# Kernel optimization log

Hardware: AMD Instinct MI355X
Metric: run time of the kernel (lower is better)

The kernel has to match this reference:

```python
import jax, jax.numpy as jnp
import numpy as np

_J6 = jnp.array([[0,0,0,0,0,1],[0,0,0,0,-1,0],[0,0,0,1,0,0],[0,0,1,0,0,0],[0,-1,0,0,0,0],[1,0,0,0,0,0]], dtype=jnp.float32)
# pairs (i,j) from combinations(range(4),2)
_PI = jnp.array([0,0,0,1,1,2])
_PJ = jnp.array([1,2,3,2,3,3])

def exterior(p1, p2):
    # p1, p2: [B,T,H,4] -> Plucker line coords [B,T,H,6], L2-normalized
    L = p1[..., _PI] * p2[..., _PJ] - p1[..., _PJ] * p2[..., _PI]
    n = jnp.clip(jnp.linalg.norm(L, axis=-1, keepdims=True), 1e-12)
    return L / n

def setup_inputs() -> dict:
    key = jax.random.key(0)
    ks = jax.random.split(key, 8)
    B, T, D, H = 2, 2048, 1024, 16
    pd = 4
    s = 0.02
    return {
        "x": jax.random.normal(ks[0], (B, T, D), jnp.float32),
        "w_qkv": jax.random.normal(ks[1], (3 * D, D), jnp.float32) * s,
        "b_qkv": jnp.zeros((3 * D,), jnp.float32),
        "w1_write": jax.random.normal(ks[2], (pd * H, D), jnp.float32) * s,
        "w2_write": jax.random.normal(ks[3], (pd * H, D), jnp.float32) * s,
        "w1_read": jax.random.normal(ks[4], (pd * H, D), jnp.float32) * s,
        "w2_read": jax.random.normal(ks[5], (pd * H, D), jnp.float32) * s,
        "w_out": jax.random.normal(ks[6], (D, D), jnp.float32) * s,
        "b_out": jnp.zeros((D,), jnp.float32),
        "decay_logits": jnp.full((H,), 4.6, jnp.float32),
        "bias_scale": jnp.full((H,), 0.1, jnp.float32),
    }

def reference(x, w_qkv, b_qkv, w1_write, w2_write, w1_read, w2_read, w_out, b_out, decay_logits, bias_scale):
    B, T, D = x.shape
    H = decay_logits.shape[0]
    dh = D // H
    pd = w1_write.shape[0] // H
    scale = dh ** -0.5

    qkv = (x @ w_qkv.T + b_qkv).reshape(B, T, 3, H, dh)
    qkv = jnp.transpose(qkv, (2, 0, 3, 1, 4))  # [3,B,H,T,dh]
    q, k, v = qkv[0], qkv[1], qkv[2]
    std_logits = jnp.einsum('bhqd,bhkd->bhqk', q, k) * scale

    x_prev = jnp.concatenate([jnp.zeros((B, 1, D), x.dtype), x[:, :-1]], axis=1)
    w1 = (x_prev @ w1_write.T).reshape(B, T, H, pd)
    w2 = (x @ w2_write.T).reshape(B, T, H, pd)
    write_lines = exterior(w1, w2)  # [B,T,H,6]
    r1 = (x @ w1_read.T).reshape(B, T, H, pd)
    r2 = (x @ w2_read.T).reshape(B, T, H, pd)
    read_lines = exterior(r1, r2)

    J_write = jnp.einsum('bthi,ij->bthj', write_lines, _J6)
    incidence = jnp.einsum('bqhp,bkhp->bhqk', read_lines, J_write)  # [B,H,T,T]

    decays = jax.nn.sigmoid(decay_logits)  # [H]
    pos = jnp.arange(T, dtype=x.dtype)
    diffs = pos[:, None] - pos[None, :]  # [T,T], q - k
    past = diffs > 0
    diffs_pos = jnp.where(past, diffs, 0.0)
    weights = (decays[:, None, None] ** diffs_pos[None]) * past[None].astype(x.dtype)  # [H,T,T]

    bias = incidence * weights[None] * bias_scale[None, :, None, None]
    logits = std_logits + bias
    causal_mask = diffs < 0  # k > q -> masked
    logits = jnp.where(causal_mask[None, None], -jnp.inf, logits)
    attn = jax.nn.softmax(logits, axis=-1)
    out = jnp.einsum('bhqk,bhkd->bqhd', attn, v).reshape(B, T, D)
    return out @ w_out.T + b_out
```

## Files before the change

kernel.cpp:

```cpp
#include <hip/hip_runtime.h>
#include <hip/hip_bf16.h>

using bhalf = __hip_bfloat16;
typedef __bf16 bf16x8 __attribute__((ext_vector_type(8)));
typedef float f32x4 __attribute__((ext_vector_type(4)));

#define B_DIM 2
#define T_DIM 2048
#define D_DIM 1024
#define H_DIM 16
#define DH 64

struct bh8 { bhalf v[8]; };
struct bh4 { bhalf v[4]; };

__device__ __forceinline__ bf16x8 load_bf16x8(const bhalf* p) {
    return __builtin_bit_cast(bf16x8, *(const uint4*)p);
}
__device__ __forceinline__ bf16x8 zero_bf16x8() {
    uint4 z; z.x = 0; z.y = 0; z.z = 0; z.w = 0;
    return __builtin_bit_cast(bf16x8, z);
}
__device__ __forceinline__ void stage8_cvt(bhalf* dst, const float* src) {
    float4 a = *(const float4*)src;
    float4 b = *(const float4*)(src + 4);
    bh8 t;
    t.v[0] = __float2bfloat16(a.x); t.v[1] = __float2bfloat16(a.y);
    t.v[2] = __float2bfloat16(a.z); t.v[3] = __float2bfloat16(a.w);
    t.v[4] = __float2bfloat16(b.x); t.v[5] = __float2bfloat16(b.y);
    t.v[6] = __float2bfloat16(b.z); t.v[7] = __float2bfloat16(b.w);
    *(uint4*)dst = __builtin_bit_cast(uint4, t);
}

#define GLD16(gp, lp) __builtin_amdgcn_global_load_lds( \
    (const __attribute__((address_space(1))) void*)(gp), \
    (__attribute__((address_space(3))) void*)(lp), 16, 0, 0)

#define SX  4194304
#define SW  3145728
#define SL  65536
#define SO  1048576
__global__ __launch_bounds__(256) void cvt_all(
    const float* __restrict__ x, const float* __restrict__ wqkv,
    const float* __restrict__ w1w, const float* __restrict__ w2w,
    const float* __restrict__ w1r, const float* __restrict__ w2r,
    const float* __restrict__ wout,
    bhalf* __restrict__ xbf, bhalf* __restrict__ wcat, bhalf* __restrict__ woutbf)
{
    int i = (blockIdx.x * 256 + threadIdx.x) * 8;
    if (i < SX) { stage8_cvt(xbf + i, x + i); return; }
    i -= SX;
    if (i < SW) { stage8_cvt(wcat + i, wqkv + i); return; }
    i -= SW;
    if (i < SL) { stage8_cvt(wcat + SW + i, w1w + i); return; }
    i -= SL;
    if (i < SL) { stage8_cvt(wcat + SW + SL + i, w2w + i); return; }
    i -= SL;
    if (i < SL) { stage8_cvt(wcat + SW + 2 * SL + i, w1r + i); return; }
    i -= SL;
    if (i < SL) { stage8_cvt(wcat + SW + 3 * SL + i, w2r + i); return; }
    i -= SL;
    if (i < SO) { stage8_cvt(woutbf + i, wout + i); }
}

__device__ __forceinline__ void gemm128_mainloop(
    const bhalf* __restrict__ A, const bhalf* __restrict__ B, int K,
    bhalf* As, bhalf* Bs, f32x4 acc[4][4])
{
    const int tid = threadIdx.x;
    const int wave = tid >> 6, lane = tid & 63;
    const int ln = lane & 15, lg = lane >> 4;
    const int wr = (wave >> 1) * 64, wc = (wave & 1) * 64;
    const int lrow = lane >> 3;
    const int lcol = (lane & 7) * 8;

    for (int kt = 0; kt < K; kt += 64) {
        __syncthreads();
#pragma unroll
        for (int i = 0; i < 4; ++i) {
            int idx = __builtin_amdgcn_readfirstlane(wave * 4 + i);
            GLD16(A + (size_t)(idx * 8 + lrow) * K + kt + lcol, As + idx * 512);
            GLD16(B + (size_t)(idx * 8 + lrow) * K + kt + lcol, Bs + idx * 512);
        }
        __syncthreads();
#pragma unroll
        for (int ks = 0; ks < 2; ++ks) {
            bf16x8 af[4], bfr[4];
#pragma unroll
            for (int mt = 0; mt < 4; ++mt)
                af[mt] = load_bf16x8(As + (wr + mt * 16 + ln) * 64 + ks * 32 + lg * 8);
#pragma unroll
            for (int nt = 0; nt < 4; ++nt)
                bfr[nt] = load_bf16x8(Bs + (wc + nt * 16 + ln) * 64 + ks * 32 + lg * 8);
#pragma unroll
            for (int mt = 0; mt < 4; ++mt)
#pragma unroll
                for (int nt = 0; nt < 4; ++nt)
                    acc[mt][nt] = __builtin_amdgcn_mfma_f32_16x16x32_bf16(af[mt], bfr[nt], acc[mt][nt], 0, 0, 0);
        }
    }
}

__global__ __launch_bounds__(256) void qkv_lines_gemm128(
    const bhalf* __restrict__ x, const bhalf* __restrict__ wcat, const float* __restrict__ bqkv,
    bhalf* __restrict__ qo, bhalf* __restrict__ ko, bhalf* __restrict__ vt,
    float* __restrict__ proj)
{
    __shared__ bhalf As[128 * 64];
    __shared__ bhalf Bs[128 * 64];
    f32x4 acc[4][4] = {};
    gemm128_mainloop(x + (size_t)blockIdx.x * 128 * D_DIM,
                     wcat + (size_t)blockIdx.y * 128 * D_DIM, D_DIM, As, Bs, acc);
    const int wave = threadIdx.x >> 6, lane = threadIdx.x & 63;
    const int ln = lane & 15, lg = lane >> 4;
    const int wr = (wave >> 1) * 64, wc = (wave & 1) * 64;
#pragma unroll
    for (int nt = 0; nt < 4; ++nt) {
        int n = blockIdx.y * 128 + wc + nt * 16 + ln;
        int trip = n >> 10, h = (n >> 6) & 15, d = n & 63;
        float bias = (trip < 3) ? bqkv[n] : 0.f;
#pragma unroll
        for (int mt = 0; mt < 4; ++mt)
#pragma unroll
            for (int r = 0; r < 4; ++r) {
                int tok = blockIdx.x * 128 + wr + mt * 16 + lg * 4 + r;
                int b = tok >> 11, t = tok & (T_DIM - 1);
                float y = acc[mt][nt][r] + bias;
                if (trip == 0) {
                    qo[(((size_t)(b * H_DIM + h)) * T_DIM + t) * DH + d] = __float2bfloat16(y * 0.125f);
                } else if (trip == 1) {
                    ko[(((size_t)(b * H_DIM + h)) * T_DIM + t) * DH + d] = __float2bfloat16(y);
                } else if (trip == 2) {
                    vt[(((size_t)(b * H_DIM + h)) * DH + d) * T_DIM + t] = __float2bfloat16(y);
                } else {
                    proj[(size_t)tok * 256 + (n - 3072)] = y;
                }
            }
    }
}

__global__ __launch_bounds__(256) void out_gemm64(
    const bhalf* __restrict__ a, const bhalf* __restrict__ w, const float* __restrict__ bo,
    float* __restrict__ out)
{
    __shared__ bhalf As[64 * 64];
    __shared__ bhalf Bs[64 * 64];
    const int tid = threadIdx.x;
    const int wave = tid >> 6, lane = tid & 63;
    const int ln = lane & 15, lg = lane >> 4;
    const int lrow = lane >> 3;
    const int lcol = (lane & 7) * 8;
    const bhalf* A = a + (size_t)blockIdx.x * 64 * D_DIM;
    const bhalf* B = w + (size_t)blockIdx.y * 64 * D_DIM;
    f32x4 acc[4] = {};

    for (int kt = 0; kt < D_DIM; kt += 64) {
        __syncthreads();
#pragma unroll
        for (int i = 0; i < 2; ++i) {
            int idx = __builtin_amdgcn_readfirstlane(wave * 2 + i);
            GLD16(A + (size_t)(idx * 8 + lrow) * D_DIM + kt + lcol, As + idx * 512);
            GLD16(B + (size_t)(idx * 8 + lrow) * D_DIM + kt + lcol, Bs + idx * 512);
        }
        __syncthreads();
#pragma unroll
        for (int ks = 0; ks < 2; ++ks) {
            bf16x8 af = load_bf16x8(As + (wave * 16 + ln) * 64 + ks * 32 + lg * 8);
#pragma unroll
            for (int nt = 0; nt < 4; ++nt) {
                bf16x8 bfr = load_bf16x8(Bs + (nt * 16 + ln) * 64 + ks * 32 + lg * 8);
                acc[nt] = __builtin_amdgcn_mfma_f32_16x16x32_bf16(af, bfr, acc[nt], 0, 0, 0);
            }
        }
    }
#pragma unroll
    for (int nt = 0; nt < 4; ++nt) {
        int n = blockIdx.y * 64 + nt * 16 + ln;
        float bias = bo[n];
#pragma unroll
        for (int r = 0; r < 4; ++r) {
            int tok = blockIdx.x * 64 + wave * 16 + lg * 4 + r;
            out[(size_t)tok * D_DIM + n] = acc[nt][r] + bias;
        }
    }
}

__global__ __launch_bounds__(256) void build_lines(
    const float* __restrict__ proj, const float* __restrict__ bias_scale,
    const float* __restrict__ decay_logits,
    bhalf* __restrict__ read8, bhalf* __restrict__ jw8)
{
    int id = blockIdx.x * 256 + threadIdx.x;
    int tok = id >> 4, h = id & 15;
    int b = tok >> 11, t = tok & (T_DIM - 1);
    const float* pr = proj + (size_t)tok * 256;

    float p1[4], p2[4], r1[4], r2[4];
#pragma unroll
    for (int i = 0; i < 4; ++i) {
        p1[i] = (t > 0) ? pr[-256 + h * 4 + i] : 0.f;
        p2[i] = pr[64 + h * 4 + i];
        r1[i] = pr[128 + h * 4 + i];
        r2[i] = pr[192 + h * 4 + i];
    }
    float Lw[6], Lr[6];
    {
        Lw[0] = p1[0] * p2[1] - p1[1] * p2[0];
        Lw[1] = p1[0] * p2[2] - p1[2] * p2[0];
        Lw[2] = p1[0] * p2[3] - p1[3] * p2[0];
        Lw[3] = p1[1] * p2[2] - p1[2] * p2[1];
        Lw[4] = p1[1] * p2[3] - p1[3] * p2[1];
        Lw[5] = p1[2] * p2[3] - p1[3] * p2[2];
        float n2 = 0.f;
#pragma unroll
        for (int j = 0; j < 6; ++j) n2 += Lw[j] * Lw[j];
        float inv = 1.f / fmaxf(sqrtf(n2), 1e-12f);
#pragma unroll
        for (int j = 0; j < 6; ++j) Lw[j] *= inv;
    }
    {
        Lr[0] = r1[0] * r2[1] - r1[1] * r2[0];
        Lr[1] = r1[0] * r2[2] - r1[2] * r2[0];
        Lr[2] = r1[0] * r2[3] - r1[3] * r2[0];
        Lr[3] = r1[1] * r2[2] - r1[2] * r2[1];
        Lr[4] = r1[1] * r2[3] - r1[3] * r2[1];
        Lr[5] = r1[2] * r2[3] - r1[3] * r2[2];
        float n2 = 0.f;
#pragma unroll
        for (int j = 0; j < 6; ++j) n2 += Lr[j] * Lr[j];
        float inv = 1.f / fmaxf(sqrtf(n2), 1e-12f);
#pragma unroll
        for (int j = 0; j < 6; ++j) Lr[j] *= inv;
    }
    float decay = 1.f / (1.f + __expf(-decay_logits[h]));
    float l2d = log2f(decay);
    float bs = bias_scale[h] * exp2f(-(float)t * l2d);
    size_t base = (((size_t)(b * H_DIM + h)) * T_DIM + t) * 8;
    read8[base + 0] = __float2bfloat16(Lr[0]);
    read8[base + 1] = __float2bfloat16(Lr[1]);
    read8[base + 2] = __float2bfloat16(Lr[2]);
    read8[base + 3] = __float2bfloat16(Lr[3]);
    read8[base + 4] = __float2bfloat16(Lr[4]);
    read8[base + 5] = __float2bfloat16(Lr[5]);
    read8[base + 6] = __float2bfloat16(0.f);
    read8[base + 7] = __float2bfloat16(0.f);
    jw8[base + 0] = __float2bfloat16(Lw[5] * bs);
    jw8[base + 1] = __float2bfloat16(-Lw[4] * bs);
    jw8[base + 2] = __float2bfloat16(Lw[3] * bs);
    jw8[base + 3] = __float2bfloat16(Lw[2] * bs);
    jw8[base + 4] = __float2bfloat16(-Lw[1] * bs);
    jw8[base + 5] = __float2bfloat16(Lw[0] * bs);
    jw8[base + 6] = __float2bfloat16(0.f);
    jw8[base + 7] = __float2bfloat16(0.f);
}

__global__ __launch_bounds__(256) void attn_kernel(
    const bhalf* __restrict__ q, const bhalf* __restrict__ k, const bhalf* __restrict__ vt,
    const bhalf* __restrict__ read8, const bhalf* __restrict__ jw8,
    const float* __restrict__ decay_logits, bhalf* __restrict__ attn_out)
{
    __shared__ float sm[4352];
    const int wave = threadIdx.x >> 6, lane = threadIdx.x & 63;
    const int ln = lane & 15, lg = lane >> 4;
    const int h = blockIdx.y, b = blockIdx.z;
    const int qa = blockIdx.x;
    const int qb = 127 - qa;
    const int rqa = qa * 16, rqb = qb * 16;
    const size_t hb = (size_t)(b * H_DIM + h);
    const bhalf* qh = q + hb * T_DIM * DH;
    const bhalf* kh = k + hb * T_DIM * DH;
    const bhalf* vh = vt + hb * DH * T_DIM;
    const bhalf* r8 = read8 + hb * T_DIM * 8;
    const bhalf* j8 = jw8 + hb * T_DIM * 8;

    bhalf* plA = (bhalf*)sm + wave * 640;
    bhalf* plB = (bhalf*)sm + 2560 + wave * 640;

    bf16x8 zf = zero_bf16x8();
    bf16x8 qA0 = load_bf16x8(qh + (rqa + ln) * DH + lg * 8);
    bf16x8 qA1 = load_bf16x8(qh + (rqa + ln) * DH + 32 + lg * 8);
    bf16x8 qB0 = load_bf16x8(qh + (rqb + ln) * DH + lg * 8);
    bf16x8 qB1 = load_bf16x8(qh + (rqb + ln) * DH + 32 + lg * 8);
    bf16x8 rfA = (lane < 16) ? load_bf16x8(r8 + (size_t)(rqa + ln) * 8) : zf;
    bf16x8 rfB = (lane < 16) ? load_bf16x8(r8 + (size_t)(rqb + ln) * 8) : zf;

    float decay = 1.f / (1.f + __expf(-decay_logits[h]));
    float l2d = log2f(decay);
    const float LOG2E = 1.44269504f;
    float aqA[4], aqB[4];
#pragma unroll
    for (int r = 0; r < 4; ++r) {
        aqA[r] = exp2f((float)(rqa + lg * 4 + r) * l2d);
        aqB[r] = exp2f((float)(rqb + lg * 4 + r) * l2d);
    }

    f32x4 oA[4] = {}, oB[4] = {};
    float lpA[4] = {0.f, 0.f, 0.f, 0.f}, lpB[4] = {0.f, 0.f, 0.f, 0.f};

    const int nca = qa / 2 + 1, ncb = qb / 2 + 1;
    for (int c = wave; c < ncb; c += 4) {
        const int kb = c * 32;
        bf16x8 k00 = load_bf16x8(kh + (kb + ln) * DH + lg * 8);
        bf16x8 k01 = load_bf16x8(kh + (kb + ln) * DH + 32 + lg * 8);
        bf16x8 k10 = load_bf16x8(kh + (kb + 16 + ln) * DH + lg * 8);
        bf16x8 k11 = load_bf16x8(kh + (kb + 16 + ln) * DH + 32 + lg * 8);
        bf16x8 j0 = (lane < 16) ? load_bf16x8(j8 + (size_t)(kb + ln) * 8) : zf;
        bf16x8 j1 = (lane < 16) ? load_bf16x8(j8 + (size_t)(kb + 16 + ln) * 8) : zf;
        bf16x8 vf0 = load_bf16x8(vh + (size_t)(ln) * T_DIM + kb + lg * 8);
        bf16x8 vf1 = load_bf16x8(vh + (size_t)(16 + ln) * T_DIM + kb + lg * 8);
        bf16x8 vf2 = load_bf16x8(vh + (size_t)(32 + ln) * T_DIM + kb + lg * 8);
        bf16x8 vf3 = load_bf16x8(vh + (size_t)(48 + ln) * T_DIM + kb + lg * 8);
        const bool doA = (c < nca);

        {
            f32x4 z0 = {}, z1 = {}, i0 = {}, i1 = {};
            z0 = __builtin_amdgcn_mfma_f32_16x16x32_bf16(qB0, k00, z0, 0, 0, 0);
            z0 = __builtin_amdgcn_mfma_f32_16x16x32_bf16(qB1, k01, z0, 0, 0, 0);
            i0 = __builtin_amdgcn_mfma_f32_16x16x32_bf16(rfB, j0, i0, 0, 0, 0);
            z1 = __builtin_amdgcn_mfma_f32_16x16x32_bf16(qB0, k10, z1, 0, 0, 0);
            z1 = __builtin_amdgcn_mfma_f32_16x16x32_bf16(qB1, k11, z1, 0, 0, 0);
            i1 = __builtin_amdgcn_mfma_f32_16x16x32_bf16(rfB, j1, i1, 0, 0, 0);
#pragma unroll
            for (int r = 0; r < 4; ++r) {
                int diff0 = rqb + lg * 4 + r - (kb + ln);
                float s0 = z0[r] + ((diff0 > 0) ? i0[r] * aqB[r] : 0.f);
                float p0 = (diff0 < 0) ? 0.f : exp2f(s0 * LOG2E);
                plB[(lg * 4 + r) * 40 + ln] = __float2bfloat16(p0);
                int diff1 = diff0 - 16;
                float s1 = z1[r] + ((diff1 > 0) ? i1[r] * aqB[r] : 0.f);
                float p1 = (diff1 < 0) ? 0.f : exp2f(s1 * LOG2E);
                plB[(lg * 4 + r) * 40 + 16 + ln] = __float2bfloat16(p1);
                lpB[r] += p0 + p1;
            }
        }
        if (doA) {
            f32x4 z0 = {}, z1 = {}, i0 = {}, i1 = {};
            z0 = __builtin_amdgcn_mfma_f32_16x16x32_bf16(qA0, k00, z0, 0, 0, 0);
            z0 = __builtin_amdgcn_mfma_f32_16x16x32_bf16(qA1, k01, z0, 0, 0, 0);
            i0 = __builtin_amdgcn_mfma_f32_16x16x32_bf16(rfA, j0, i0, 0, 0, 0);
            z1 = __builtin_amdgcn_mfma_f32_16x16x32_bf16(qA0, k10, z1, 0, 0, 0);
            z1 = __builtin_amdgcn_mfma_f32_16x16x32_bf16(qA1, k11, z1, 0, 0, 0);
            i1 = __builtin_amdgcn_mfma_f32_16x16x32_bf16(rfA, j1, i1, 0, 0, 0);
#pragma unroll
            for (int r = 0; r < 4; ++r) {
                int diff0 = rqa + lg * 4 + r - (kb + ln);
                float s0 = z0[r] + ((diff0 > 0) ? i0[r] * aqA[r] : 0.f);
                float p0 = (diff0 < 0) ? 0.f : exp2f(s0 * LOG2E);
                plA[(lg * 4 + r) * 40 + ln] = __float2bfloat16(p0);
                int diff1 = diff0 - 16;
                float s1 = z1[r] + ((diff1 > 0) ? i1[r] * aqA[r] : 0.f);
                float p1 = (diff1 < 0) ? 0.f : exp2f(s1 * LOG2E);
                plA[(lg * 4 + r) * 40 + 16 + ln] = __float2bfloat16(p1);
                lpA[r] += p0 + p1;
            }
        }
        __asm__ volatile("s_waitcnt lgkmcnt(0)" ::: "memory");
        {
            bf16x8 pf = load_bf16x8(plB + ln * 40 + lg * 8);
            oB[0] = __builtin_amdgcn_mfma_f32_16x16x32_bf16(pf, vf0, oB[0], 0, 0, 0);
            oB[1] = __builtin_amdgcn_mfma_f32_16x16x32_bf16(pf, vf1, oB[1], 0, 0, 0);
            oB[2] = __builtin_amdgcn_mfma_f32_16x16x32_bf16(pf, vf2, oB[2], 0, 0, 0);
            oB[3] = __builtin_amdgcn_mfma_f32_16x16x32_bf16(pf, vf3, oB[3], 0, 0, 0);
        }
        if (doA) {
            bf16x8 pf = load_bf16x8(plA + ln * 40 + lg * 8);
            oA[0] = __builtin_amdgcn_mfma_f32_16x16x32_bf16(pf, vf0, oA[0], 0, 0, 0);
            oA[1] = __builtin_amdgcn_mfma_f32_16x16x32_bf16(pf, vf1, oA[1], 0, 0, 0);
            oA[2] = __builtin_amdgcn_mfma_f32_16x16x32_bf16(pf, vf2, oA[2], 0, 0, 0);
            oA[3] = __builtin_amdgcn_mfma_f32_16x16x32_bf16(pf, vf3, oA[3], 0, 0, 0);
        }
    }

#pragma unroll
    for (int r = 0; r < 4; ++r) {
#pragma unroll
        for (int off = 1; off < 16; off <<= 1) {
            lpA[r] += __shfl_xor(lpA[r], off, 16);
            lpB[r] += __shfl_xor(lpB[r], off, 16);
        }
    }

    const int row = threadIdx.x >> 4;
    const int c4 = (threadIdx.x & 15) * 4;

    __syncthreads();
#pragma unroll
    for (int r = 0; r < 4; ++r) {
        if (ln == 0) sm[wave * 1088 + (lg * 4 + r) * 68 + 64] = lpA[r];
#pragma unroll
        for (int nt = 0; nt < 4; ++nt)
            sm[wave * 1088 + (lg * 4 + r) * 68 + nt * 16 + ln] = oA[nt][r];
    }
    __syncthreads();
    {
        float l = 0.f;
#pragma unroll
        for (int w = 0; w < 4; ++w) l += sm[w * 1088 + row * 68 + 64];
        float4 acc = {0.f, 0.f, 0.f, 0.f};
#pragma unroll
        for (int w = 0; w < 4; ++w) {
            float4 t = *(const float4*)&sm[w * 1088 + row * 68 + c4];
            acc.x += t.x; acc.y += t.y; acc.z += t.z; acc.w += t.w;
        }
        float invl = 1.f / l;
        bh4 pk;
        pk.v[0] = __float2bfloat16(acc.x * invl);
        pk.v[1] = __float2bfloat16(acc.y * invl);
        pk.v[2] = __float2bfloat16(acc.z * invl);
        pk.v[3] = __float2bfloat16(acc.w * invl);
        size_t tok = (size_t)b * T_DIM + rqa + row;
        *(uint2*)&attn_out[tok * D_DIM + h * DH + c4] = __builtin_bit_cast(uint2, pk);
    }

    __syncthreads();
#pragma unroll
    for (int r = 0; r < 4; ++r) {
        if (ln == 0) sm[wave * 1088 + (lg * 4 + r) * 68 + 64] = lpB[r];
#pragma unroll
        for (int nt = 0; nt < 4; ++nt)
            sm[wave * 1088 + (lg * 4 + r) * 68 + nt * 16 + ln] = oB[nt][r];
    }
    __syncthreads();
    {
        float l = 0.f;
#pragma unroll
        for (int w = 0; w < 4; ++w) l += sm[w * 1088 + row * 68 + 64];
        float4 acc = {0.f, 0.f, 0.f, 0.f};
#pragma unroll
        for (int w = 0; w < 4; ++w) {
            float4 t = *(const float4*)&sm[w * 1088 + row * 68 + c4];
            acc.x += t.x; acc.y += t.y; acc.z += t.z; acc.w += t.w;
        }
        float invl = 1.f / l;
        bh4 pk;
        pk.v[0] = __float2bfloat16(acc.x * invl);
        pk.v[1] = __float2bfloat16(acc.y * invl);
        pk.v[2] = __float2bfloat16(acc.z * invl);
        pk.v[3] = __float2bfloat16(acc.w * invl);
        size_t tok = (size_t)b * T_DIM + rqb + row;
        *(uint2*)&attn_out[tok * D_DIM + h * DH + c4] = __builtin_bit_cast(uint2, pk);
    }
}

extern "C" void kernel_launch(void* const* d_in, const int* in_sizes, int n_in,
                              void* d_out, int out_size, void* d_ws, size_t ws_size,
                              hipStream_t stream)
{
    const float* x    = (const float*)d_in[0];
    const float* wqkv = (const float*)d_in[1];
    const float* bqkv = (const float*)d_in[2];
    const float* w1w  = (const float*)d_in[3];
    const float* w2w  = (const float*)d_in[4];
    const float* w1r  = (const float*)d_in[5];
    const float* w2r  = (const float*)d_in[6];
    const float* wout = (const float*)d_in[7];
    const float* bout = (const float*)d_in[8];
    const float* dlog = (const float*)d_in[9];
    const float* bsc  = (const float*)d_in[10];
    float* out = (float*)d_out;

    char* ws = (char*)d_ws;
    bhalf* qb    = (bhalf*)(ws);
    bhalf* kbuf  = (bhalf*)(ws + 8388608);
    bhalf* vtb   = (bhalf*)(ws + 16777216);
    bhalf* r8    = (bhalf*)(ws + 25165824);
    bhalf* j8    = (bhalf*)(ws + 26214400);
    float* proj  = (float*)(ws + 27262976);
    bhalf* ao    = (bhalf*)(ws + 31457280);
    bhalf* woutbf = (bhalf*)(ws + 39845888);

    bhalf* xbf  = (bhalf*)d_out;
    bhalf* wcat = (bhalf*)((char*)d_out + 8388608);

    cvt_all<<<4224, 256, 0, stream>>>(x, wqkv, w1w, w2w, w1r, w2r, wout, xbf, wcat, woutbf);
    qkv_lines_gemm128<<<dim3(32, 26), 256, 0, stream>>>(xbf, wcat, bqkv, qb, kbuf, vtb, proj);
    build_lines<<<256, 256, 0, stream>>>(proj, bsc, dlog, r8, j8);
    attn_kernel<<<dim3(64, H_DIM, B_DIM), 256, 0, stream>>>(qb, kbuf, vtb, r8, j8, dlog, ao);
    out_gemm64<<<dim3(64, 16), 256, 0, stream>>>(ao, woutbf, bout, out);
}
```

Measured before the change: 309.9 us.

## Specialize diagonal tiles, interleave key rows, and vectorize V-transpose stores

Result: faster. 302.6 us (-2.3%).

```diff
diff --git a/kernel.cpp b/kernel.cpp
--- a/kernel.cpp
+++ b/kernel.cpp
@@ -3,6 +3,7 @@
 
 using bhalf = __hip_bfloat16;
 typedef __bf16 bf16x8 __attribute__((ext_vector_type(8)));
+typedef __bf16 bf16x2 __attribute__((ext_vector_type(2)));
 typedef float f32x4 __attribute__((ext_vector_type(4)));
 
 #define B_DIM 2
@@ -114,28 +115,48 @@
     const int wave = threadIdx.x >> 6, lane = threadIdx.x & 63;
     const int ln = lane & 15, lg = lane >> 4;
     const int wr = (wave >> 1) * 64, wc = (wave & 1) * 64;
-#pragma unroll
-    for (int nt = 0; nt < 4; ++nt) {
-        int n = blockIdx.y * 128 + wc + nt * 16 + ln;
-        int trip = n >> 10, h = (n >> 6) & 15, d = n & 63;
-        float bias = (trip < 3) ? bqkv[n] : 0.f;
-#pragma unroll
-        for (int mt = 0; mt < 4; ++mt)
-#pragma unroll
-            for (int r = 0; r < 4; ++r) {
-                int tok = blockIdx.x * 128 + wr + mt * 16 + lg * 4 + r;
-                int b = tok >> 11, t = tok & (T_DIM - 1);
-                float y = acc[mt][nt][r] + bias;
-                if (trip == 0) {
-                    qo[(((size_t)(b * H_DIM + h)) * T_DIM + t) * DH + d] = __float2bfloat16(y * 0.125f);
-                } else if (trip == 1) {
-                    ko[(((size_t)(b * H_DIM + h)) * T_DIM + t) * DH + d] = __float2bfloat16(y);
-                } else if (trip == 2) {
-                    vt[(((size_t)(b * H_DIM + h)) * DH + d) * T_DIM + t] = __float2bfloat16(y);
-                } else {
-                    proj[(size_t)tok * 256 + (n - 3072)] = y;
+    const int trip = (blockIdx.y * 128) >> 10;
+
+    if (trip == 2) {
+#pragma unroll
+        for (int nt = 0; nt < 4; ++nt) {
+            int n = blockIdx.y * 128 + wc + nt * 16 + ln;
+            float bias = bqkv[n];
+            int h = (n >> 6) & 15, d = n & 63;
+#pragma unroll
+            for (int mt = 0; mt < 4; ++mt) {
+                int tok0 = blockIdx.x * 128 + wr + mt * 16 + lg * 4;
+                int b = tok0 >> 11, t0 = tok0 & (T_DIM - 1);
+                bh4 pk;
+#pragma unroll
+                for (int r = 0; r < 4; ++r)
+                    pk.v[r] = __float2bfloat16(acc[mt][nt][r] + bias);
+                *(uint2*)&vt[(((size_t)(b * H_DIM + h)) * DH + d) * T_DIM + t0] =
+                    __builtin_bit_cast(uint2, pk);
+            }
+        }
+    } else {
+#pragma unroll
+        for (int nt = 0; nt < 4; ++nt) {
+            int n = blockIdx.y * 128 + wc + nt * 16 + ln;
+            int h = (n >> 6) & 15, d = n & 63;
+            float bias = (trip < 3) ? bqkv[n] : 0.f;
+#pragma unroll
+            for (int mt = 0; mt < 4; ++mt)
+#pragma unroll
+                for (int r = 0; r < 4; ++r) {
+                    int tok = blockIdx.x * 128 + wr + mt * 16 + lg * 4 + r;
+                    int b = tok >> 11, t = tok & (T_DIM - 1);
+                    float y = acc[mt][nt][r] + bias;
+                    if (trip == 0) {
+                        qo[(((size_t)(b * H_DIM + h)) * T_DIM + t) * DH + d] = __float2bfloat16(y * 0.125f);
+                    } else if (trip == 1) {
+                        ko[(((size_t)(b * H_DIM + h)) * T_DIM + t) * DH + d] = __float2bfloat16(y);
+                    } else {
+                        proj[(size_t)tok * 256 + (n - 3072)] = y;
+                    }
                 }
-            }
+        }
     }
 }
 
@@ -254,6 +275,34 @@
     jw8[base + 7] = __float2bfloat16(0.f);
 }
 
+template<bool DIAG>
+__device__ __forceinline__ void tile_step(
+    const f32x4& z0, const f32x4& z1, const f32x4& i0, const f32x4& i1,
+    int rq, int kb, const float* aq, int lg, int ln, bhalf* pl, float* lp)
+{
+    const float LOG2E = 1.44269504f;
+#pragma unroll
+    for (int r = 0; r < 4; ++r) {
+        float p0, p1;
+        if (DIAG) {
+            int diff0 = rq + lg * 4 + r - (kb + 2 * ln);
+            float s0 = z0[r] + ((diff0 > 0) ? i0[r] * aq[r] : 0.f);
+            p0 = (diff0 < 0) ? 0.f : exp2f(s0 * LOG2E);
+            int diff1 = diff0 - 1;
+            float s1 = z1[r] + ((diff1 > 0) ? i1[r] * aq[r] : 0.f);
+            p1 = (diff1 < 0) ? 0.f : exp2f(s1 * LOG2E);
+        } else {
+            p0 = exp2f(fmaf(i0[r], aq[r], z0[r]) * LOG2E);
+            p1 = exp2f(fmaf(i1[r], aq[r], z1[r]) * LOG2E);
+        }
+        bf16x2 h2;
+        h2.x = (__bf16)p0;
+        h2.y = (__bf16)p1;
+        *(unsigned int*)&pl[(lg * 4 + r) * 40 + 2 * ln] = __builtin_bit_cast(unsigned int, h2);
+        lp[r] += p0 + p1;
+    }
+}
+
 __global__ __launch_bounds__(256) void attn_kernel(
     const bhalf* __restrict__ q, const bhalf* __restrict__ k, const bhalf* __restrict__ vt,
     const bhalf* __restrict__ read8, const bhalf* __restrict__ jw8,
@@ -286,7 +335,6 @@
 
     float decay = 1.f / (1.f + __expf(-decay_logits[h]));
     float l2d = log2f(decay);
-    const float LOG2E = 1.44269504f;
     float aqA[4], aqB[4];
 #pragma unroll
     for (int r = 0; r < 4; ++r) {
@@ -300,12 +348,12 @@
     const int nca = qa / 2 + 1, ncb = qb / 2 + 1;
     for (int c = wave; c < ncb; c += 4) {
         const int kb = c * 32;
-        bf16x8 k00 = load_bf16x8(kh + (kb + ln) * DH + lg * 8);
-        bf16x8 k01 = load_bf16x8(kh + (kb + ln) * DH + 32 + lg * 8);
-        bf16x8 k10 = load_bf16x8(kh + (kb + 16 + ln) * DH + lg * 8);
-        bf16x8 k11 = load_bf16x8(kh + (kb + 16 + ln) * DH + 32 + lg * 8);
-        bf16x8 j0 = (lane < 16) ? load_bf16x8(j8 + (size_t)(kb + ln) * 8) : zf;
-        bf16x8 j1 = (lane < 16) ? load_bf16x8(j8 + (size_t)(kb + 16 + ln) * 8) : zf;
+        bf16x8 k00 = load_bf16x8(kh + (kb + 2 * ln) * DH + lg * 8);
+        bf16x8 k01 = load_bf16x8(kh + (kb + 2 * ln) * DH + 32 + lg * 8);
+        bf16x8 k10 = load_bf16x8(kh + (kb + 2 * ln + 1) * DH + lg * 8);
+        bf16x8 k11 = load_bf16x8(kh + (kb + 2 * ln + 1) * DH + 32 + lg * 8);
+        bf16x8 j0 = (lane < 16) ? load_bf16x8(j8 + (size_t)(kb + 2 * ln) * 8) : zf;
+        bf16x8 j1 = (lane < 16) ? load_bf16x8(j8 + (size_t)(kb + 2 * ln + 1) * 8) : zf;
         bf16x8 vf0 = load_bf16x8(vh + (size_t)(ln) * T_DIM + kb + lg * 8);
         bf16x8 vf1 = load_bf16x8(vh + (size_t)(16 + ln) * T_DIM + kb + lg * 8);
         bf16x8 vf2 = load_bf16x8(vh + (size_t)(32 + ln) * T_DIM + kb + lg * 8);
@@ -320,18 +368,8 @@
             z1 = __builtin_amdgcn_mfma_f32_16x16x32_bf16(qB0, k10, z1, 0, 0, 0);
             z1 = __builtin_amdgcn_mfma_f32_16x16x32_bf16(qB1, k11, z1, 0, 0, 0);
             i1 = __builtin_amdgcn_mfma_f32_16x16x32_bf16(rfB, j1, i1, 0, 0, 0);
-#pragma unroll
-            for (int r = 0; r < 4; ++r) {
-                int diff0 = rqb + lg * 4 + r - (kb + ln);
-                float s0 = z0[r] + ((diff0 > 0) ? i0[r] * aqB[r] : 0.f);
-                float p0 = (diff0 < 0) ? 0.f : exp2f(s0 * LOG2E);
-                plB[(lg * 4 + r) * 40 + ln] = __float2bfloat16(p0);
-                int diff1 = diff0 - 16;
-                float s1 = z1[r] + ((diff1 > 0) ? i1[r] * aqB[r] : 0.f);
-                float p1 = (diff1 < 0) ? 0.f : exp2f(s1 * LOG2E);
-                plB[(lg * 4 + r) * 40 + 16 + ln] = __float2bfloat16(p1);
-                lpB[r] += p0 + p1;
-            }
+            if (c == ncb - 1) tile_step<true >(z0, z1, i0, i1, rqb, kb, aqB, lg, ln, plB, lpB);
+            else              tile_step<false>(z0, z1, i0, i1, rqb, kb, aqB, lg, ln, plB, lpB);
         }
         if (doA) {
             f32x4 z0 = {}, z1 = {}, i0 = {}, i1 = {};
@@ -341,18 +379,8 @@
             z1 = __builtin_amdgcn_mfma_f32_16x16x32_bf16(qA0, k10, z1, 0, 0, 0);
             z1 = __builtin_amdgcn_mfma_f32_16x16x32_bf16(qA1, k11, z1, 0, 0, 0);
             i1 = __builtin_amdgcn_mfma_f32_16x16x32_bf16(rfA, j1, i1, 0, 0, 0);
-#pragma unroll
-            for (int r = 0; r < 4; ++r) {
-                int diff0 = rqa + lg * 4 + r - (kb + ln);
-                float s0 = z0[r] + ((diff0 > 0) ? i0[r] * aqA[r] : 0.f);
-                float p0 = (diff0 < 0) ? 0.f : exp2f(s0 * LOG2E);
-                plA[(lg * 4 + r) * 40 + ln] = __float2bfloat16(p0);
-                int diff1 = diff0 - 16;
-                float s1 = z1[r] + ((diff1 > 0) ? i1[r] * aqA[r] : 0.f);
-                float p1 = (diff1 < 0) ? 0.f : exp2f(s1 * LOG2E);
-                plA[(lg * 4 + r) * 40 + 16 + ln] = __float2bfloat16(p1);
-                lpA[r] += p0 + p1;
-            }
+            if (c == nca - 1) tile_step<true >(z0, z1, i0, i1, rqa, kb, aqA, lg, ln, plA, lpA);
+            else              tile_step<false>(z0, z1, i0, i1, rqa, kb, aqA, lg, ln, plA, lpA);
         }
         __asm__ volatile("s_waitcnt lgkmcnt(0)" ::: "memory");
         {
```
